# Kernel optimization log

Measured on AMD Instinct MI355X. Metric: run time of the kernel, lower is better.

The kernel has to match this reference:

```python
import jax, jax.numpy as jnp
import numpy as np

B, T, D = 4, 2048, 1024
H, DH = 16, 64
GH = H * DH  # == D here
SCALE = DH ** -0.5
LN_EPS = 1e-5


def setup_inputs() -> dict:
    key = jax.random.key(0)
    ks = jax.random.split(key, 8)
    x = jax.random.normal(ks[0], (B, T, D), dtype=jnp.float32)
    attn_mask = jax.random.uniform(ks[1], (T, T), dtype=jnp.float32)
    # LayerNorm params
    gamma = jnp.ones((D,), jnp.float32)
    beta = jnp.zeros((D,), jnp.float32)
    # projection weights, stored (in, out) so y = x @ W
    Wq = jax.random.normal(ks[2], (D, GH), jnp.float32) * (D ** -0.5)
    Wk = jax.random.normal(ks[3], (D, GH), jnp.float32) * (D ** -0.5)
    Wv = jax.random.normal(ks[4], (D, GH), jnp.float32) * (D ** -0.5)
    Wo = jax.random.normal(ks[5], (GH, D), jnp.float32) * (GH ** -0.5)
    bo = jnp.zeros((D,), jnp.float32)
    return {"x": x, "attn_mask": attn_mask, "gamma": gamma, "beta": beta,
            "Wq": Wq, "Wk": Wk, "Wv": Wv, "Wo": Wo, "bo": bo}


def reference(x, attn_mask, gamma, beta, Wq, Wk, Wv, Wo, bo):
    # LayerNorm over last dim
    mu = jnp.mean(x, axis=-1, keepdims=True)
    var = jnp.mean((x - mu) ** 2, axis=-1, keepdims=True)
    xn = (x - mu) * jax.lax.rsqrt(var + LN_EPS) * gamma + beta
    # QKV projections (bias=False), reshape to [B, H, T, DH]
    split = lambda y: y.reshape(B, T, H, DH).transpose(0, 2, 1, 3)
    q = split(xn @ Wq)
    k = split(xn @ Wk)
    v = split(xn @ Wv)
    # scores scaled then MULTIPLICATIVELY masked (post-scale)
    scores = jnp.einsum('bhqd,bhkd->bhqk', q, k) * SCALE
    scores = scores * attn_mask  # broadcast [T,T] over [B,H,T,T]
    probs = jax.nn.softmax(scores, axis=-1)  # dropout p=0 -> identity
    av = jnp.einsum('bhqk,bhkd->bhqd', probs, v)
    av = av.transpose(0, 2, 1, 3).reshape(B, T, GH)
    return av @ Wo + bo
```

## Files before the change

kernel.cpp:

```cpp
#include <hip/hip_runtime.h>

typedef unsigned short u16;
typedef unsigned int u32;
typedef __bf16 bf16x8 __attribute__((ext_vector_type(8)));
typedef float f32x4 __attribute__((ext_vector_type(4)));

#define AS1 __attribute__((address_space(1)))
#define AS3 __attribute__((address_space(3)))

#define SWZB(x) ((x) ^ ((((x) >> 7) & 7) << 4))

__device__ __forceinline__ float bf2f(u16 u) {
    union { u32 i; float f; } v; v.i = ((u32)u) << 16; return v.f;
}
__device__ __forceinline__ u16 f2bf(float f) {
    union { float f; u32 i; } v; v.f = f;
    u32 i = v.i;
    u32 r = (i + 0x7fffu + ((i >> 16) & 1u)) >> 16;
    return (u16)r;
}
__device__ __forceinline__ float blo(u32 u) {
    union { u32 i; float f; } v; v.i = u << 16; return v.f;
}
__device__ __forceinline__ float bhi(u32 u) {
    union { u32 i; float f; } v; v.i = u & 0xFFFF0000u; return v.f;
}
__device__ __forceinline__ u32 cvtpk_bf16(float lo, float hi) {
    u32 r;
    asm("v_cvt_pk_bf16_f32 %0, %1, %2" : "=v"(r) : "v"(lo), "v"(hi));
    return r;
}
__device__ __forceinline__ float fexp2(float x) {
    float r;
    asm("v_exp_f32 %0, %1" : "=v"(r) : "v"(x));
    return r;
}
__device__ __forceinline__ void gload_lds16(const u16* src, u16* dst) {
    __builtin_amdgcn_global_load_lds((const AS1 void*)src, (AS3 void*)dst, 16, 0, 0);
}

__global__ __launch_bounds__(256) void prep_kernel(
    const float* __restrict__ x, const float* __restrict__ g,
    const float* __restrict__ bb, u16* __restrict__ xn,
    const float* __restrict__ mask, u16* __restrict__ maskb,
    const float* __restrict__ Wq, const float* __restrict__ Wk,
    const float* __restrict__ Wv, const float* __restrict__ Wo,
    u16* __restrict__ WT, u16* __restrict__ WoT) {
    __shared__ __align__(16) char lds[64 * 65 * 2];
    int bid = blockIdx.x;
    int tid = threadIdx.x;
    if (bid < 1024) {
        u16 (*t)[65] = (u16(*)[65])lds;
        int z = bid >> 8, rem = bid & 255;
        int by = rem >> 4, bx = rem & 15;
        const float* in = (z == 0) ? Wq : (z == 1) ? Wk : (z == 2) ? Wv : Wo;
        u16* out = (z < 3) ? WT + (size_t)z * 1024 * 1024 : WoT;
        float scale = (z == 0) ? 0.18033688f : 1.0f;
        int c = tid & 63, r0 = tid >> 6;
        int ib = by * 64, jb = bx * 64;
        #pragma unroll
        for (int r = r0; r < 64; r += 4)
            t[r][c] = f2bf(in[(size_t)(ib + r) * 1024 + jb + c] * scale);
        __syncthreads();
        #pragma unroll
        for (int r = r0; r < 64; r += 4) out[(size_t)(jb + r) * 1024 + ib + c] = t[c][r];
    } else if (bid < 5120) {
        int i = (bid - 1024) * 256 + tid;
        float4 v = *(const float4*)&mask[(size_t)i * 4];
        ushort4 o;
        o.x = f2bf(v.x); o.y = f2bf(v.y); o.z = f2bf(v.z); o.w = f2bf(v.w);
        *(ushort4*)&maskb[(size_t)i * 4] = o;
    } else {
        float* red = (float*)lds;
        int row = bid - 5120;
        const float* xr = x + (size_t)row * 1024;
        float4 v = *(const float4*)&xr[tid * 4];
        float f0 = v.x, f1 = v.y, f2 = v.z, f3 = v.w;
        float s = f0 + f1 + f2 + f3;
        float sq = f0 * f0 + f1 * f1 + f2 * f2 + f3 * f3;
        #pragma unroll
        for (int m = 1; m < 64; m <<= 1) { s += __shfl_xor(s, m, 64); sq += __shfl_xor(sq, m, 64); }
        int wid = tid >> 6, lane = tid & 63;
        if (lane == 0) { red[wid] = s; red[4 + wid] = sq; }
        __syncthreads();
        s = red[0] + red[1] + red[2] + red[3];
        sq = red[4] + red[5] + red[6] + red[7];
        float mu = s * (1.f / 1024.f);
        float var = sq * (1.f / 1024.f) - mu * mu;
        float rs = rsqrtf(var + 1e-5f);
        float4 gv = *(const float4*)&g[tid * 4];
        float4 bv = *(const float4*)&bb[tid * 4];
        ushort4 o;
        o.x = f2bf((f0 - mu) * rs * gv.x + bv.x);
        o.y = f2bf((f1 - mu) * rs * gv.y + bv.y);
        o.z = f2bf((f2 - mu) * rs * gv.z + bv.z);
        o.w = f2bf((f3 - mu) * rs * gv.w + bv.w);
        *(ushort4*)&xn[(size_t)row * 1024 + tid * 4] = o;
    }
}

__global__ __launch_bounds__(256) void gemm_bt(const u16* __restrict__ A,
                                               const u16* __restrict__ BT,
                                               u16* __restrict__ C16,
                                               float* __restrict__ C32,
                                               const float* __restrict__ bias,
                                               int K, int ldc, int ext, int nbx,
                                               u16* __restrict__ vTout) {
    __shared__ __align__(16) u16 lA[128 * 32];
    __shared__ __align__(16) u16 lB[128 * 32];
    int bid = blockIdx.x;
    int xcd = bid & 7, loc = bid >> 3;
    int npx = nbx >> 3;
    int n0 = (xcd * npx + loc % npx) * 128;
    int m0 = (loc / npx) * 128;
    int tid = threadIdx.x, lane = tid & 63, wid = tid >> 6;
    int wr = wid >> 1, wc = wid & 1;
    int l4 = lane >> 4, l15 = lane & 15;

    f32x4 acc[4][4] = {};
    int NT = K >> 5;

    auto stage = [&](int kt) {
        int k0 = kt << 5;
        #pragma unroll
        for (int i = 0; i < 2; ++i) {
            int j = wid * 2 + i;
            int row = j * 16 + (lane >> 2);
            int ch = (lane & 3) * 8;
            gload_lds16(A + (size_t)(m0 + row) * K + k0 + ch, &lA[j * 512]);
            gload_lds16(BT + (size_t)(n0 + row) * K + k0 + ch, &lB[j * 512]);
        }
    };
    stage(0);
    for (int kt = 0; kt < NT; ++kt) {
        __syncthreads();
        bf16x8 af[4], bfr[4];
        #pragma unroll
        for (int i = 0; i < 4; ++i) {
            af[i]  = *(const bf16x8*)&lA[(wr * 64 + i * 16 + l15) * 32 + l4 * 8];
            bfr[i] = *(const bf16x8*)&lB[(wc * 64 + i * 16 + l15) * 32 + l4 * 8];
        }
        __syncthreads();
        if (kt + 1 < NT) stage(kt + 1);
        #pragma unroll
        for (int i = 0; i < 4; ++i)
            #pragma unroll
            for (int j = 0; j < 4; ++j)
                acc[i][j] = __builtin_amdgcn_mfma_f32_16x16x32_bf16(af[i], bfr[j], acc[i][j], 0, 0, 0);
    }
    bool vblk = (vTout != nullptr) && (n0 >= 2048);
    #pragma unroll
    for (int j = 0; j < 4; ++j) {
        int col = n0 + wc * 64 + j * 16 + l15;
        if (vblk) {
            int hd = col - 2048;
            #pragma unroll
            for (int i = 0; i < 4; ++i) {
                int trow = m0 + wr * 64 + i * 16 + l4 * 4;
                int bidx = trow >> 11, t = trow & 2047;
                ushort4 pk;
                pk.x = f2bf(acc[i][j][0]);
                pk.y = f2bf(acc[i][j][1]);
                pk.z = f2bf(acc[i][j][2]);
                pk.w = f2bf(acc[i][j][3]);
                *(ushort4*)&vTout[(size_t)(bidx * 1024 + hd) * 2048 + t] = pk;
            }
        } else {
            float bv = ext ? bias[col] : 0.f;
            #pragma unroll
            for (int i = 0; i < 4; ++i) {
                #pragma unroll
                for (int r = 0; r < 4; ++r) {
                    int row = m0 + wr * 64 + i * 16 + l4 * 4 + r;
                    float val = acc[i][j][r] + bv;
                    if (ext) C32[(size_t)row * ldc + col] = val;
                    else     C16[(size_t)row * ldc + col] = f2bf(val);
                }
            }
        }
    }
}

__global__ __launch_bounds__(256) void attn_kernel(const u16* __restrict__ qkv,
                                                   const u16* __restrict__ vT,
                                                   const u16* __restrict__ maskb,
                                                   u16* __restrict__ av) {
    __shared__ __align__(16) u16 lK[2][64 * 64];
    __shared__ __align__(16) u16 lV[2][64 * 64];
    int qt = blockIdx.x, bh = blockIdx.y;
    int b = bh >> 4, h = bh & 15;
    int tid = threadIdx.x, lane = tid & 63, wid = tid >> 6;
    int l4 = lane >> 4, l15 = lane & 15;
    int qw = qt * 128 + wid * 32;

    const u16* qb0 = qkv + (size_t)(b * 2048 + qw + l15) * 2048 + h * 64;
    const u16* qb1 = qb0 + (size_t)16 * 2048;
    bf16x8 qf00 = *(const bf16x8*)&qb0[l4 * 8];
    bf16x8 qf01 = *(const bf16x8*)&qb0[32 + l4 * 8];
    bf16x8 qf10 = *(const bf16x8*)&qb1[l4 * 8];
    bf16x8 qf11 = *(const bf16x8*)&qb1[32 + l4 * 8];
    const u16* mrow0 = maskb + (size_t)(qw + l15) * 2048 + 8 * l4;
    const u16* mrow1 = mrow0 + (size_t)16 * 2048;

    f32x4 o0[4] = {}, o1[4] = {};
    float lsum0 = 0.f, lsum1 = 0.f;

    int c0 = tid, c1 = 256 + tid;
    auto pmap = [](int g) {
        return (g & 32) + 4 * ((g >> 3) & 3) + (g & 3) + ((g & 4) << 2);
    };
    int kd0 = SWZB(pmap(c0 >> 3) * 128 + (c0 & 7) * 16);
    int kd1 = SWZB(pmap(c1 >> 3) * 128 + (c1 & 7) * 16);
    int vd0 = SWZB((c0 >> 3) * 128 + (c0 & 7) * 16);
    int vd1 = SWZB((c1 >> 3) * 128 + (c1 & 7) * 16);
    const u16* ksrc0 = qkv + (size_t)(b * 2048 + (c0 >> 3)) * 2048 + 1024 + h * 64 + (c0 & 7) * 8;
    const u16* ksrc1 = qkv + (size_t)(b * 2048 + (c1 >> 3)) * 2048 + 1024 + h * 64 + (c1 & 7) * 8;
    const u16* vsrc0 = vT + (size_t)(bh * 64 + (c0 >> 3)) * 2048 + (c0 & 7) * 8;
    const u16* vsrc1 = vT + (size_t)(bh * 64 + (c1 >> 3)) * 2048 + (c1 & 7) * 8;

    auto loadKV = [&](int t, bf16x8& K0, bf16x8& K1, bf16x8& V0, bf16x8& V1) {
        size_t ko = (size_t)t * (64 * 2048);
        int vo = t * 64;
        K0 = *(const bf16x8*)(ksrc0 + ko);
        K1 = *(const bf16x8*)(ksrc1 + ko);
        V0 = *(const bf16x8*)(vsrc0 + vo);
        V1 = *(const bf16x8*)(vsrc1 + vo);
    };

    union PU { u32 u[4]; bf16x8 v; };

    auto body = [&](int t, int pbuf,
                    bf16x8& nK0, bf16x8& nK1, bf16x8& nV0, bf16x8& nV1,
                    bf16x8& fK0, bf16x8& fK1, bf16x8& fV0, bf16x8& fV1) {
        int k0 = t * 64;
        uint4 mua0 = *(const uint4*)(mrow0 + k0);
        uint4 mub0 = *(const uint4*)(mrow0 + k0 + 32);
        uint4 mua1 = *(const uint4*)(mrow1 + k0);
        uint4 mub1 = *(const uint4*)(mrow1 + k0 + 32);
        f32x4 mm0[4], mm1[4];
        mm0[0] = f32x4{blo(mua0.x), bhi(mua0.x), blo(mua0.y), bhi(mua0.y)};
        mm0[1] = f32x4{blo(mua0.z), bhi(mua0.z), blo(mua0.w), bhi(mua0.w)};
        mm0[2] = f32x4{blo(mub0.x), bhi(mub0.x), blo(mub0.y), bhi(mub0.y)};
        mm0[3] = f32x4{blo(mub0.z), bhi(mub0.z), blo(mub0.w), bhi(mub0.w)};
        mm1[0] = f32x4{blo(mua1.x), bhi(mua1.x), blo(mua1.y), bhi(mua1.y)};
        mm1[1] = f32x4{blo(mua1.z), bhi(mua1.z), blo(mua1.w), bhi(mua1.w)};
        mm1[2] = f32x4{blo(mub1.x), bhi(mub1.x), blo(mub1.y), bhi(mub1.y)};
        mm1[3] = f32x4{blo(mub1.z), bhi(mub1.z), blo(mub1.w), bhi(mub1.w)};
        const char* Kb = (const char*)lK[pbuf];
        f32x4 s0[4] = {}, s1[4] = {};
        __builtin_amdgcn_s_setprio(1);
        #pragma unroll
        for (int fj = 0; fj < 4; ++fj) {
            bf16x8 kf0 = *(const bf16x8*)(Kb + SWZB((fj * 16 + l15) * 128 + l4 * 16));
            bf16x8 kf1 = *(const bf16x8*)(Kb + SWZB((fj * 16 + l15) * 128 + 64 + l4 * 16));
            s0[fj] = __builtin_amdgcn_mfma_f32_16x16x32_bf16(kf0, qf00, s0[fj], 0, 0, 0);
            s0[fj] = __builtin_amdgcn_mfma_f32_16x16x32_bf16(kf1, qf01, s0[fj], 0, 0, 0);
            s1[fj] = __builtin_amdgcn_mfma_f32_16x16x32_bf16(kf0, qf10, s1[fj], 0, 0, 0);
            s1[fj] = __builtin_amdgcn_mfma_f32_16x16x32_bf16(kf1, qf11, s1[fj], 0, 0, 0);
        }
        __builtin_amdgcn_s_setprio(0);
        PU pa0[2], pa1[2];
        #pragma unroll
        for (int fj = 0; fj < 4; ++fj) {
            float p0 = fexp2(s0[fj][0] * mm0[fj][0]);
            float p1 = fexp2(s0[fj][1] * mm0[fj][1]);
            float p2 = fexp2(s0[fj][2] * mm0[fj][2]);
            float p3 = fexp2(s0[fj][3] * mm0[fj][3]);
            lsum0 += (p0 + p1) + (p2 + p3);
            int ks = fj >> 1, hf = (fj & 1) * 2;
            pa0[ks].u[hf]     = cvtpk_bf16(p0, p1);
            pa0[ks].u[hf + 1] = cvtpk_bf16(p2, p3);
        }
        #pragma unroll
        for (int fj = 0; fj < 4; ++fj) {
            float p0 = fexp2(s1[fj][0] * mm1[fj][0]);
            float p1 = fexp2(s1[fj][1] * mm1[fj][1]);
            float p2 = fexp2(s1[fj][2] * mm1[fj][2]);
            float p3 = fexp2(s1[fj][3] * mm1[fj][3]);
            lsum1 += (p0 + p1) + (p2 + p3);
            int ks = fj >> 1, hf = (fj & 1) * 2;
            pa1[ks].u[hf]     = cvtpk_bf16(p0, p1);
            pa1[ks].u[hf + 1] = cvtpk_bf16(p2, p3);
        }
        if (t + 1 < 32) {
            char* Kn = (char*)lK[pbuf ^ 1];
            char* Vn = (char*)lV[pbuf ^ 1];
            *(bf16x8*)(Kn + kd0) = nK0;
            *(bf16x8*)(Kn + kd1) = nK1;
            *(bf16x8*)(Vn + vd0) = nV0;
            *(bf16x8*)(Vn + vd1) = nV1;
        }
        if (t + 2 < 32) loadKV(t + 2, fK0, fK1, fV0, fV1);
        const char* Vb = (const char*)lV[pbuf];
        __builtin_amdgcn_s_setprio(1);
        #pragma unroll
        for (int ks = 0; ks < 2; ++ks) {
            #pragma unroll
            for (int fj = 0; fj < 4; ++fj) {
                bf16x8 vf = *(const bf16x8*)(Vb + SWZB((fj * 16 + l15) * 128 + ks * 64 + l4 * 16));
                o0[fj] = __builtin_amdgcn_mfma_f32_16x16x32_bf16(pa0[ks].v, vf, o0[fj], 0, 0, 0);
                o1[fj] = __builtin_amdgcn_mfma_f32_16x16x32_bf16(pa1[ks].v, vf, o1[fj], 0, 0, 0);
            }
        }
        __builtin_amdgcn_s_setprio(0);
        __syncthreads();
    };

    bf16x8 ka0, ka1, va0, va1, kb0, kb1, vb0, vb1;
    loadKV(0, ka0, ka1, va0, va1);
    *(bf16x8*)((char*)lK[0] + kd0) = ka0;
    *(bf16x8*)((char*)lK[0] + kd1) = ka1;
    *(bf16x8*)((char*)lV[0] + vd0) = va0;
    *(bf16x8*)((char*)lV[0] + vd1) = va1;
    loadKV(1, kb0, kb1, vb0, vb1);
    __syncthreads();
    for (int t = 0; t < 32; t += 2) {
        body(t,     0, kb0, kb1, vb0, vb1, ka0, ka1, va0, va1);
        body(t + 1, 1, ka0, ka1, va0, va1, kb0, kb1, vb0, vb1);
    }

    lsum0 += __shfl_xor(lsum0, 16, 64);
    lsum0 += __shfl_xor(lsum0, 32, 64);
    lsum1 += __shfl_xor(lsum1, 16, 64);
    lsum1 += __shfl_xor(lsum1, 32, 64);
    float den0[4], den1[4];
    #pragma unroll
    for (int r = 0; r < 4; ++r) {
        den0[r] = __shfl(lsum0, l4 * 4 + r, 64);
        den1[r] = __shfl(lsum1, l4 * 4 + r, 64);
    }
    #pragma unroll
    for (int fj = 0; fj < 4; ++fj) {
        #pragma unroll
        for (int r = 0; r < 4; ++r) {
            int col = h * 64 + fj * 16 + l15;
            av[(size_t)(b * 2048 + qw + l4 * 4 + r) * 1024 + col]      = f2bf(o0[fj][r] / den0[r]);
            av[(size_t)(b * 2048 + qw + 16 + l4 * 4 + r) * 1024 + col] = f2bf(o1[fj][r] / den1[r]);
        }
    }
}

extern "C" void kernel_launch(void* const* d_in, const int* in_sizes, int n_in,
                              void* d_out, int out_size, void* d_ws, size_t ws_size,
                              hipStream_t stream) {
    (void)in_sizes; (void)n_in; (void)out_size; (void)ws_size;
    const float* x     = (const float*)d_in[0];
    const float* mask  = (const float*)d_in[1];
    const float* gamma = (const float*)d_in[2];
    const float* beta  = (const float*)d_in[3];
    const float* Wq    = (const float*)d_in[4];
    const float* Wk    = (const float*)d_in[5];
    const float* Wv    = (const float*)d_in[6];
    const float* Wo    = (const float*)d_in[7];
    const float* bo    = (const float*)d_in[8];

    char* ws = (char*)d_ws;
    u16* xn    = (u16*)(ws);
    u16* WT    = (u16*)(ws + 16777216);
    u16* WoT   = (u16*)(ws + 23068672);
    u16* qkvb  = (u16*)(ws + 25165824);
    u16* vT    = (u16*)(ws + 58720256);
    u16* maskb = (u16*)(ws + 75497472);
    u16* av = xn;

    dim3 tb(256);
    prep_kernel<<<13312, tb, 0, stream>>>(x, gamma, beta, xn, mask, maskb,
                                          Wq, Wk, Wv, Wo, WT, WoT);
    gemm_bt<<<24 * 64, tb, 0, stream>>>(xn, WT, qkvb, nullptr, nullptr, 1024, 2048, 0, 24, vT);
    attn_kernel<<<dim3(16, 64), tb, 0, stream>>>(qkvb, vT, maskb, av);
    gemm_bt<<<8 * 64, tb, 0, stream>>>(av, WoT, nullptr, (float*)d_out, bo, 1024, 1024, 1, 8, nullptr);
}
```

Measured before the change: 238.6 us.

## Process 64 query rows per wave to double K/V tile reuse in attention

Each wave now handles four 16-row query groups (two 32-row blocks, 1024 rows apart) instead of two, and the grid is halved to 8x64 blocks. Every K/V tile staged in shared memory is reused across twice as many queries, halving global K/V traffic and barrier count per query. The prefetch is also simplified from two-ahead register double buffering to a one-ahead load. The costs are higher register pressure, lower occupancy, only 512 blocks to fill the GPU, and less latency hiding for the global loads.

```diff
diff --git a/kernel.cpp b/kernel.cpp
--- a/kernel.cpp
+++ b/kernel.cpp
@@ -191,19 +191,24 @@
     int b = bh >> 4, h = bh & 15;
     int tid = threadIdx.x, lane = tid & 63, wid = tid >> 6;
     int l4 = lane >> 4, l15 = lane & 15;
-    int qw = qt * 128 + wid * 32;
-
-    const u16* qb0 = qkv + (size_t)(b * 2048 + qw + l15) * 2048 + h * 64;
-    const u16* qb1 = qb0 + (size_t)16 * 2048;
-    bf16x8 qf00 = *(const bf16x8*)&qb0[l4 * 8];
-    bf16x8 qf01 = *(const bf16x8*)&qb0[32 + l4 * 8];
-    bf16x8 qf10 = *(const bf16x8*)&qb1[l4 * 8];
-    bf16x8 qf11 = *(const bf16x8*)&qb1[32 + l4 * 8];
-    const u16* mrow0 = maskb + (size_t)(qw + l15) * 2048 + 8 * l4;
-    const u16* mrow1 = mrow0 + (size_t)16 * 2048;
-
-    f32x4 o0[4] = {}, o1[4] = {};
-    float lsum0 = 0.f, lsum1 = 0.f;
+    int qw1 = qt * 128 + wid * 32;
+    int qw2 = qw1 + 1024;
+
+    const u16* qbA = qkv + (size_t)(b * 2048 + qw1 + l15) * 2048 + h * 64;
+    const u16* qbB = qbA + (size_t)16 * 2048;
+    const u16* qbC = qkv + (size_t)(b * 2048 + qw2 + l15) * 2048 + h * 64;
+    const u16* qbD = qbC + (size_t)16 * 2048;
+    bf16x8 qfA0 = *(const bf16x8*)&qbA[l4 * 8], qfA1 = *(const bf16x8*)&qbA[32 + l4 * 8];
+    bf16x8 qfB0 = *(const bf16x8*)&qbB[l4 * 8], qfB1 = *(const bf16x8*)&qbB[32 + l4 * 8];
+    bf16x8 qfC0 = *(const bf16x8*)&qbC[l4 * 8], qfC1 = *(const bf16x8*)&qbC[32 + l4 * 8];
+    bf16x8 qfD0 = *(const bf16x8*)&qbD[l4 * 8], qfD1 = *(const bf16x8*)&qbD[32 + l4 * 8];
+    const u16* mrowA = maskb + (size_t)(qw1 + l15) * 2048 + 8 * l4;
+    const u16* mrowB = mrowA + (size_t)16 * 2048;
+    const u16* mrowC = maskb + (size_t)(qw2 + l15) * 2048 + 8 * l4;
+    const u16* mrowD = mrowC + (size_t)16 * 2048;
+
+    f32x4 oA[4] = {}, oB[4] = {}, oC[4] = {}, oD[4] = {};
+    float lsA = 0.f, lsB = 0.f, lsC = 0.f, lsD = 0.f;
 
     int c0 = tid, c1 = 256 + tid;
     auto pmap = [](int g) {
@@ -218,79 +223,102 @@
     const u16* vsrc0 = vT + (size_t)(bh * 64 + (c0 >> 3)) * 2048 + (c0 & 7) * 8;
     const u16* vsrc1 = vT + (size_t)(bh * 64 + (c1 >> 3)) * 2048 + (c1 & 7) * 8;
 
-    auto loadKV = [&](int t, bf16x8& K0, bf16x8& K1, bf16x8& V0, bf16x8& V1) {
-        size_t ko = (size_t)t * (64 * 2048);
-        int vo = t * 64;
-        K0 = *(const bf16x8*)(ksrc0 + ko);
-        K1 = *(const bf16x8*)(ksrc1 + ko);
-        V0 = *(const bf16x8*)(vsrc0 + vo);
-        V1 = *(const bf16x8*)(vsrc1 + vo);
-    };
-
     union PU { u32 u[4]; bf16x8 v; };
 
-    auto body = [&](int t, int pbuf,
-                    bf16x8& nK0, bf16x8& nK1, bf16x8& nV0, bf16x8& nV1,
-                    bf16x8& fK0, bf16x8& fK1, bf16x8& fV0, bf16x8& fV1) {
+    auto loadMM = [&](const u16* mrow, int k0, f32x4* mm) {
+        uint4 mua = *(const uint4*)(mrow + k0);
+        uint4 mub = *(const uint4*)(mrow + k0 + 32);
+        mm[0] = f32x4{blo(mua.x), bhi(mua.x), blo(mua.y), bhi(mua.y)};
+        mm[1] = f32x4{blo(mua.z), bhi(mua.z), blo(mua.w), bhi(mua.w)};
+        mm[2] = f32x4{blo(mub.x), bhi(mub.x), blo(mub.y), bhi(mub.y)};
+        mm[3] = f32x4{blo(mub.z), bhi(mub.z), blo(mub.w), bhi(mub.w)};
+    };
+    auto expPack = [&](f32x4 (&s)[4], f32x4* mm, float& ls, PU (&pa)[2]) {
+        #pragma unroll
+        for (int fj = 0; fj < 4; ++fj) {
+            float p0 = fexp2(s[fj][0] * mm[fj][0]);
+            float p1 = fexp2(s[fj][1] * mm[fj][1]);
+            float p2 = fexp2(s[fj][2] * mm[fj][2]);
+            float p3 = fexp2(s[fj][3] * mm[fj][3]);
+            ls += (p0 + p1) + (p2 + p3);
+            int ks = fj >> 1, hf = (fj & 1) * 2;
+            pa[ks].u[hf]     = cvtpk_bf16(p0, p1);
+            pa[ks].u[hf + 1] = cvtpk_bf16(p2, p3);
+        }
+    };
+
+    {
+        bf16x8 k0r = *(const bf16x8*)ksrc0;
+        bf16x8 k1r = *(const bf16x8*)ksrc1;
+        bf16x8 v0r = *(const bf16x8*)vsrc0;
+        bf16x8 v1r = *(const bf16x8*)vsrc1;
+        *(bf16x8*)((char*)lK[0] + kd0) = k0r;
+        *(bf16x8*)((char*)lK[0] + kd1) = k1r;
+        *(bf16x8*)((char*)lV[0] + vd0) = v0r;
+        *(bf16x8*)((char*)lV[0] + vd1) = v1r;
+    }
+    __syncthreads();
+
+    for (int t = 0; t < 32; ++t) {
+        int pbuf = t & 1;
         int k0 = t * 64;
-        uint4 mua0 = *(const uint4*)(mrow0 + k0);
-        uint4 mub0 = *(const uint4*)(mrow0 + k0 + 32);
-        uint4 mua1 = *(const uint4*)(mrow1 + k0);
-        uint4 mub1 = *(const uint4*)(mrow1 + k0 + 32);
-        f32x4 mm0[4], mm1[4];
-        mm0[0] = f32x4{blo(mua0.x), bhi(mua0.x), blo(mua0.y), bhi(mua0.y)};
-        mm0[1] = f32x4{blo(mua0.z), bhi(mua0.z), blo(mua0.w), bhi(mua0.w)};
-        mm0[2] = f32x4{blo(mub0.x), bhi(mub0.x), blo(mub0.y), bhi(mub0.y)};
-        mm0[3] = f32x4{blo(mub0.z), bhi(mub0.z), blo(mub0.w), bhi(mub0.w)};
-        mm1[0] = f32x4{blo(mua1.x), bhi(mua1.x), blo(mua1.y), bhi(mua1.y)};
-        mm1[1] = f32x4{blo(mua1.z), bhi(mua1.z), blo(mua1.w), bhi(mua1.w)};
-        mm1[2] = f32x4{blo(mub1.x), bhi(mub1.x), blo(mub1.y), bhi(mub1.y)};
-        mm1[3] = f32x4{blo(mub1.z), bhi(mub1.z), blo(mub1.w), bhi(mub1.w)};
+        bf16x8 nk0, nk1, nv0, nv1;
+        if (t + 1 < 32) {
+            size_t ko = (size_t)(t + 1) * (64 * 2048);
+            int vo = (t + 1) * 64;
+            nk0 = *(const bf16x8*)(ksrc0 + ko);
+            nk1 = *(const bf16x8*)(ksrc1 + ko);
+            nv0 = *(const bf16x8*)(vsrc0 + vo);
+            nv1 = *(const bf16x8*)(vsrc1 + vo);
+        }
         const char* Kb = (const char*)lK[pbuf];
-        f32x4 s0[4] = {}, s1[4] = {};
-        __builtin_amdgcn_s_setprio(1);
-        #pragma unroll
-        for (int fj = 0; fj < 4; ++fj) {
-            bf16x8 kf0 = *(const bf16x8*)(Kb + SWZB((fj * 16 + l15) * 128 + l4 * 16));
-            bf16x8 kf1 = *(const bf16x8*)(Kb + SWZB((fj * 16 + l15) * 128 + 64 + l4 * 16));
-            s0[fj] = __builtin_amdgcn_mfma_f32_16x16x32_bf16(kf0, qf00, s0[fj], 0, 0, 0);
-            s0[fj] = __builtin_amdgcn_mfma_f32_16x16x32_bf16(kf1, qf01, s0[fj], 0, 0, 0);
-            s1[fj] = __builtin_amdgcn_mfma_f32_16x16x32_bf16(kf0, qf10, s1[fj], 0, 0, 0);
-            s1[fj] = __builtin_amdgcn_mfma_f32_16x16x32_bf16(kf1, qf11, s1[fj], 0, 0, 0);
-        }
-        __builtin_amdgcn_s_setprio(0);
-        PU pa0[2], pa1[2];
-        #pragma unroll
-        for (int fj = 0; fj < 4; ++fj) {
-            float p0 = fexp2(s0[fj][0] * mm0[fj][0]);
-            float p1 = fexp2(s0[fj][1] * mm0[fj][1]);
-            float p2 = fexp2(s0[fj][2] * mm0[fj][2]);
-            float p3 = fexp2(s0[fj][3] * mm0[fj][3]);
-            lsum0 += (p0 + p1) + (p2 + p3);
-            int ks = fj >> 1, hf = (fj & 1) * 2;
-            pa0[ks].u[hf]     = cvtpk_bf16(p0, p1);
-            pa0[ks].u[hf + 1] = cvtpk_bf16(p2, p3);
-        }
-        #pragma unroll
-        for (int fj = 0; fj < 4; ++fj) {
-            float p0 = fexp2(s1[fj][0] * mm1[fj][0]);
-            float p1 = fexp2(s1[fj][1] * mm1[fj][1]);
-            float p2 = fexp2(s1[fj][2] * mm1[fj][2]);
-            float p3 = fexp2(s1[fj][3] * mm1[fj][3]);
-            lsum1 += (p0 + p1) + (p2 + p3);
-            int ks = fj >> 1, hf = (fj & 1) * 2;
-            pa1[ks].u[hf]     = cvtpk_bf16(p0, p1);
-            pa1[ks].u[hf + 1] = cvtpk_bf16(p2, p3);
+        PU paA[2], paB[2], paC[2], paD[2];
+        {
+            f32x4 mmA[4], mmB[4];
+            loadMM(mrowA, k0, mmA);
+            loadMM(mrowB, k0, mmB);
+            f32x4 sA[4] = {}, sB[4] = {};
+            __builtin_amdgcn_s_setprio(1);
+            #pragma unroll
+            for (int fj = 0; fj < 4; ++fj) {
+                bf16x8 kf0 = *(const bf16x8*)(Kb + SWZB((fj * 16 + l15) * 128 + l4 * 16));
+                bf16x8 kf1 = *(const bf16x8*)(Kb + SWZB((fj * 16 + l15) * 128 + 64 + l4 * 16));
+                sA[fj] = __builtin_amdgcn_mfma_f32_16x16x32_bf16(kf0, qfA0, sA[fj], 0, 0, 0);
+                sA[fj] = __builtin_amdgcn_mfma_f32_16x16x32_bf16(kf1, qfA1, sA[fj], 0, 0, 0);
+                sB[fj] = __builtin_amdgcn_mfma_f32_16x16x32_bf16(kf0, qfB0, sB[fj], 0, 0, 0);
+                sB[fj] = __builtin_amdgcn_mfma_f32_16x16x32_bf16(kf1, qfB1, sB[fj], 0, 0, 0);
+            }
+            __builtin_amdgcn_s_setprio(0);
+            expPack(sA, mmA, lsA, paA);
+            expPack(sB, mmB, lsB, paB);
+        }
+        {
+            f32x4 mmC[4], mmD[4];
+            loadMM(mrowC, k0, mmC);
+            loadMM(mrowD, k0, mmD);
+            f32x4 sC[4] = {}, sD[4] = {};
+            __builtin_amdgcn_s_setprio(1);
+            #pragma unroll
+            for (int fj = 0; fj < 4; ++fj) {
+                bf16x8 kf0 = *(const bf16x8*)(Kb + SWZB((fj * 16 + l15) * 128 + l4 * 16));
+                bf16x8 kf1 = *(const bf16x8*)(Kb + SWZB((fj * 16 + l15) * 128 + 64 + l4 * 16));
+                sC[fj] = __builtin_amdgcn_mfma_f32_16x16x32_bf16(kf0, qfC0, sC[fj], 0, 0, 0);
+                sC[fj] = __builtin_amdgcn_mfma_f32_16x16x32_bf16(kf1, qfC1, sC[fj], 0, 0, 0);
+                sD[fj] = __builtin_amdgcn_mfma_f32_16x16x32_bf16(kf0, qfD0, sD[fj], 0, 0, 0);
+                sD[fj] = __builtin_amdgcn_mfma_f32_16x16x32_bf16(kf1, qfD1, sD[fj], 0, 0, 0);
+            }
+            __builtin_amdgcn_s_setprio(0);
+            expPack(sC, mmC, lsC, paC);
+            expPack(sD, mmD, lsD, paD);
         }
         if (t + 1 < 32) {
             char* Kn = (char*)lK[pbuf ^ 1];
             char* Vn = (char*)lV[pbuf ^ 1];
-            *(bf16x8*)(Kn + kd0) = nK0;
-            *(bf16x8*)(Kn + kd1) = nK1;
-            *(bf16x8*)(Vn + vd0) = nV0;
-            *(bf16x8*)(Vn + vd1) = nV1;
-        }
-        if (t + 2 < 32) loadKV(t + 2, fK0, fK1, fV0, fV1);
+            *(bf16x8*)(Kn + kd0) = nk0;
+            *(bf16x8*)(Kn + kd1) = nk1;
+            *(bf16x8*)(Vn + vd0) = nv0;
+            *(bf16x8*)(Vn + vd1) = nv1;
+        }
         const char* Vb = (const char*)lV[pbuf];
         __builtin_amdgcn_s_setprio(1);
         #pragma unroll
@@ -298,46 +326,35 @@
             #pragma unroll
             for (int fj = 0; fj < 4; ++fj) {
                 bf16x8 vf = *(const bf16x8*)(Vb + SWZB((fj * 16 + l15) * 128 + ks * 64 + l4 * 16));
-                o0[fj] = __builtin_amdgcn_mfma_f32_16x16x32_bf16(pa0[ks].v, vf, o0[fj], 0, 0, 0);
-                o1[fj] = __builtin_amdgcn_mfma_f32_16x16x32_bf16(pa1[ks].v, vf, o1[fj], 0, 0, 0);
+                oA[fj] = __builtin_amdgcn_mfma_f32_16x16x32_bf16(paA[ks].v, vf, oA[fj], 0, 0, 0);
+                oB[fj] = __builtin_amdgcn_mfma_f32_16x16x32_bf16(paB[ks].v, vf, oB[fj], 0, 0, 0);
+                oC[fj] = __builtin_amdgcn_mfma_f32_16x16x32_bf16(paC[ks].v, vf, oC[fj], 0, 0, 0);
+                oD[fj] = __builtin_amdgcn_mfma_f32_16x16x32_bf16(paD[ks].v, vf, oD[fj], 0, 0, 0);
             }
         }
         __builtin_amdgcn_s_setprio(0);
         __syncthreads();
-    };
-
-    bf16x8 ka0, ka1, va0, va1, kb0, kb1, vb0, vb1;
-    loadKV(0, ka0, ka1, va0, va1);
-    *(bf16x8*)((char*)lK[0] + kd0) = ka0;
-    *(bf16x8*)((char*)lK[0] + kd1) = ka1;
-    *(bf16x8*)((char*)lV[0] + vd0) = va0;
-    *(bf16x8*)((char*)lV[0] + vd1) = va1;
-    loadKV(1, kb0, kb1, vb0, vb1);
-    __syncthreads();
-    for (int t = 0; t < 32; t += 2) {
-        body(t,     0, kb0, kb1, vb0, vb1, ka0, ka1, va0, va1);
-        body(t + 1, 1, ka0, ka1, va0, va1, kb0, kb1, vb0, vb1);
-    }
-
-    lsum0 += __shfl_xor(lsum0, 16, 64);
-    lsum0 += __shfl_xor(lsum0, 32, 64);
-    lsum1 += __shfl_xor(lsum1, 16, 64);
-    lsum1 += __shfl_xor(lsum1, 32, 64);
-    float den0[4], den1[4];
-    #pragma unroll
-    for (int r = 0; r < 4; ++r) {
-        den0[r] = __shfl(lsum0, l4 * 4 + r, 64);
-        den1[r] = __shfl(lsum1, l4 * 4 + r, 64);
-    }
-    #pragma unroll
-    for (int fj = 0; fj < 4; ++fj) {
-        #pragma unroll
-        for (int r = 0; r < 4; ++r) {
-            int col = h * 64 + fj * 16 + l15;
-            av[(size_t)(b * 2048 + qw + l4 * 4 + r) * 1024 + col]      = f2bf(o0[fj][r] / den0[r]);
-            av[(size_t)(b * 2048 + qw + 16 + l4 * 4 + r) * 1024 + col] = f2bf(o1[fj][r] / den1[r]);
-        }
-    }
+    }
+
+    auto finish = [&](float ls, f32x4 (&o)[4], int qwrow) {
+        ls += __shfl_xor(ls, 16, 64);
+        ls += __shfl_xor(ls, 32, 64);
+        float den[4];
+        #pragma unroll
+        for (int r = 0; r < 4; ++r) den[r] = __shfl(ls, l4 * 4 + r, 64);
+        #pragma unroll
+        for (int fj = 0; fj < 4; ++fj) {
+            #pragma unroll
+            for (int r = 0; r < 4; ++r) {
+                av[(size_t)(b * 2048 + qwrow + l4 * 4 + r) * 1024 + h * 64 + fj * 16 + l15] =
+                    f2bf(o[fj][r] / den[r]);
+            }
+        }
+    };
+    finish(lsA, oA, qw1);
+    finish(lsB, oB, qw1 + 16);
+    finish(lsC, oC, qw2);
+    finish(lsD, oD, qw2 + 16);
 }
 
 extern "C" void kernel_launch(void* const* d_in, const int* in_sizes, int n_in,
@@ -367,6 +384,6 @@
     prep_kernel<<<13312, tb, 0, stream>>>(x, gamma, beta, xn, mask, maskb,
                                           Wq, Wk, Wv, Wo, WT, WoT);
     gemm_bt<<<24 * 64, tb, 0, stream>>>(xn, WT, qkvb, nullptr, nullptr, 1024, 2048, 0, 24, vT);
-    attn_kernel<<<dim3(16, 64), tb, 0, stream>>>(qkvb, vT, maskb, av);
+    attn_kernel<<<dim3(8, 64), tb, 0, stream>>>(qkvb, vT, maskb, av);
     gemm_bt<<<8 * 64, tb, 0, stream>>>(av, WoT, nullptr, (float*)d_out, bo, 1024, 1024, 1, 8, nullptr);
 }
```

New measurement: 306.4 us. 1.28x slower.
